# Optimization experiments

Measured on AMD Instinct MI355X. Metric: run time of the kernel, lower is better.

The kernel has to match this reference:

```python
import jax, jax.numpy as jnp
import numpy as np

B, S, T = 32, 2048, 768
NH, DH, DHID = 8, 96, 384  # num_heads, head_dim, hidden_dim=4*head_dim


def setup_inputs() -> dict:
    key = jax.random.key(0)
    k = jax.random.split(key, 7)
    token_embeddings = jax.random.normal(k[0], (B, S, T), dtype=jnp.float32)
    attention_mask = jnp.ones((B, S), dtype=jnp.float32)
    # per-head Linear params, stacked on a leading head axis (PyTorch default-ish init scale)
    P_w = jax.random.normal(k[1], (NH, T, DH), dtype=jnp.float32) * (1.0 / np.sqrt(T))
    P_b = jax.random.normal(k[2], (NH, DH), dtype=jnp.float32) * 0.01
    W1_w = jax.random.normal(k[3], (NH, DH, DHID), dtype=jnp.float32) * (1.0 / np.sqrt(DH))
    W1_b = jax.random.normal(k[4], (NH, DHID), dtype=jnp.float32) * 0.01
    W2_w = jax.random.normal(k[5], (NH, DHID, DH), dtype=jnp.float32) * (1.0 / np.sqrt(DHID))
    W2_b = jax.random.normal(k[6], (NH, DH), dtype=jnp.float32) * 0.01
    return {
        'token_embeddings': token_embeddings,
        'attention_mask': attention_mask,
        'P_w': P_w, 'P_b': P_b,
        'W1_w': W1_w, 'W1_b': W1_b,
        'W2_w': W2_w, 'W2_b': W2_b,
    }


def reference(token_embeddings, attention_mask, P_w, P_b, W1_w, W1_b, W2_w, W2_b):
    # Batched over heads instead of the original Python loop; same math per head.
    # H_i = P_i(H): (B, NH, S, DH)
    Hi = jnp.einsum('bst,htd->bhsd', token_embeddings, P_w) + P_b[None, :, None, :]
    # A_i = W2_i(relu(W1_i(H_i))): (B, NH, S, DH)
    A = jax.nn.relu(jnp.einsum('bhsd,hde->bhse', Hi, W1_w) + W1_b[None, :, None, :])
    A = jnp.einsum('bhse,hed->bhsd', A, W2_w) + W2_b[None, :, None, :]
    # masked softmax over the sequence axis (log(mask) adds -inf at padded tokens)
    log_mask = jnp.log(attention_mask)[:, None, :, None]  # (B,1,S,1)
    A = jax.nn.softmax(A + log_mask, axis=2)
    # weighted sum over tokens: (B, NH, DH)
    v = jnp.sum(Hi * A, axis=2)
    # concat heads -> (B, NH*DH) == (B, sentence_dim)
    return v.reshape(v.shape[0], NH * DH)
```

## Files before the change

kernel.cpp:

```cpp
#include <hip/hip_runtime.h>
#include <cstdint>
#include <cstddef>

#define Bsz   32
#define Ssz   2048
#define Tsz   768
#define NH    8
#define DH    96
#define DHID  384
#define Ncols (NH*DH)

using u16 = unsigned short;
typedef __bf16 bf16x8 __attribute__((ext_vector_type(8)));
typedef __bf16 bf16x4 __attribute__((ext_vector_type(4)));
typedef float  f32x4  __attribute__((ext_vector_type(4)));

__device__ __forceinline__ u16 f2bn(float f) {
  __bf16 h = (__bf16)f;
  return __builtin_bit_cast(u16, h);
}
__device__ __forceinline__ float b2f(u16 u) {
  return __builtin_bit_cast(float, (uint32_t)u << 16);
}

typedef const __attribute__((address_space(1))) void* gas_t;
typedef __attribute__((address_space(3))) void* las_t;
__device__ __forceinline__ void gload16(const void* g, void* s) {
  __builtin_amdgcn_global_load_lds((gas_t)g, (las_t)s, 16, 0, 0);
}

__global__ __launch_bounds__(256) void k_cvt(const float* __restrict__ e,
                                             u16* __restrict__ o)
{
  size_t t = (size_t)blockIdx.x * 256 + threadIdx.x;
  #pragma unroll
  for (int it = 0; it < 3; ++it) {
    size_t i = (t + (size_t)it * 2097152) * 8;
    float4 v0 = *reinterpret_cast<const float4*>(e + i);
    float4 v1 = *reinterpret_cast<const float4*>(e + i + 4);
    bf16x8 p;
    p[0] = (__bf16)v0.x; p[1] = (__bf16)v0.y; p[2] = (__bf16)v0.z; p[3] = (__bf16)v0.w;
    p[4] = (__bf16)v1.x; p[5] = (__bf16)v1.y; p[6] = (__bf16)v1.z; p[7] = (__bf16)v1.w;
    *reinterpret_cast<bf16x8*>(o + i) = p;
  }
}

__global__ __launch_bounds__(256) void k_pack(const float* __restrict__ Pw,
    const float* __restrict__ W1w, const float* __restrict__ W2w,
    u16* __restrict__ B1t, u16* __restrict__ W1t, u16* __restrict__ W2t)
{
  int i = blockIdx.x * 256 + threadIdx.x;
  if (i < 589824) {
    int n = i / 768, k = i % 768;
    int h = n / 96, d = n % 96;
    B1t[i] = f2bn(Pw[(size_t)h*73728 + (size_t)k*96 + d]);
  } else if (i < 589824 + 294912) {
    int j = i - 589824;
    int h = j / 36864, r = j % 36864;
    int n = r / 96, k = r % 96;
    W1t[j] = f2bn(W1w[(size_t)h*36864 + (size_t)k*384 + n]);
  } else if (i < 589824 + 2*294912) {
    int q = i - 589824 - 294912;
    int h = q / 36864, r = q % 36864;
    int n = r / 384, k = r % 384;
    W2t[q] = f2bn(W2w[(size_t)h*36864 + (size_t)k*96 + n]);
  }
}

__global__ __launch_bounds__(256) void k_gemm1(const u16* __restrict__ embb,
    const u16* __restrict__ B1t, const float* __restrict__ Pb, u16* __restrict__ Hi)
{
  __shared__ u16 As[128*64];
  __shared__ u16 Bs[128*64];
  const int tid  = threadIdx.x;
  const int lane = tid & 63;
  const int w    = tid >> 6;
  const int wr = w >> 1, wc = w & 1;
  const int L = blockIdx.x;
  const int widx = (L & 7) * 384 + (L >> 3);
  const int bm = widx / 6, bn = widx % 6;
  const int l15 = lane & 15, lg = lane >> 4;

  const int lrow = lane >> 3;
  const int lchk = (lane & 7) ^ lrow;

  f32x4 acc[4][4] = {};

  #pragma unroll 1
  for (int kt = 0; kt < 12; ++kt) {
    const int k0 = kt * 64;
    #pragma unroll
    for (int i = 0; i < 4; ++i) {
      const int r8 = (w*4 + i)*8;
      gload16(embb + (size_t)(bm*128 + r8 + lrow)*Tsz + k0 + lchk*8,
              &As[r8*64]);
      gload16(B1t  + (size_t)(bn*128 + r8 + lrow)*Tsz + k0 + lchk*8,
              &Bs[r8*64]);
    }
    __syncthreads();

    __builtin_amdgcn_s_setprio(1);
    #pragma unroll
    for (int kk = 0; kk < 2; ++kk) {
      const int clog = kk*4 + lg;
      bf16x8 b[4];
      #pragma unroll
      for (int c = 0; c < 4; ++c) {
        const int Rb = wc*64 + c*16 + l15;
        b[c] = *reinterpret_cast<const bf16x8*>(&Bs[Rb*64 + (clog ^ (Rb & 7))*8]);
      }
      bf16x8 a[4];
      #pragma unroll
      for (int m = 0; m < 4; ++m) {
        const int R = wr*64 + m*16 + l15;
        a[m] = *reinterpret_cast<const bf16x8*>(&As[R*64 + (clog ^ (R & 7))*8]);
      }
      #pragma unroll
      for (int m = 0; m < 4; ++m)
        #pragma unroll
        for (int c = 0; c < 4; ++c)
          acc[m][c] = __builtin_amdgcn_mfma_f32_16x16x32_bf16(a[m], b[c], acc[m][c], 0, 0, 0);
    }
    __builtin_amdgcn_s_setprio(0);
    __syncthreads();
  }

  #pragma unroll
  for (int c = 0; c < 4; ++c) {
    int col = bn*128 + wc*64 + c*16 + l15;
    float bias = Pb[col];
    #pragma unroll
    for (int m = 0; m < 4; ++m) {
      int row0 = bm*128 + wr*64 + m*16 + lg*4;
      #pragma unroll
      for (int j = 0; j < 4; ++j)
        Hi[(size_t)(row0 + j)*Ncols + col] = f2bn(acc[m][c][j] + bias);
    }
  }
}

__global__ __launch_bounds__(256, 2) void k_gemm1_fb(const float* __restrict__ emb,
    const u16* __restrict__ B1t, const float* __restrict__ Pb, u16* __restrict__ Hi)
{
  __shared__ u16 As[2][128*64];
  __shared__ u16 Bs[2][128*64];
  const int tid  = threadIdx.x;
  const int lane = tid & 63;
  const int w    = tid >> 6;
  const int wr = w >> 1, wc = w & 1;
  const int L = blockIdx.x;
  const int widx = (L & 7) * 384 + (L >> 3);
  const int bm = widx / 6, bn = widx % 6;
  const int l15 = lane & 15, lg = lane >> 4;

  const int srow   = lane >> 3;
  const int schunk = lane & 7;
  const int wchunk = schunk ^ srow;

  bf16x8 pa[4];
  bf16x8 pb[4];

  auto load_tile = [&](int kt) {
    const int k0 = kt * 64;
    #pragma unroll
    for (int i = 0; i < 4; ++i) {
      const int row = w*32 + i*8 + srow;
      const float* src = emb + (size_t)(bm*128 + row)*Tsz + k0 + schunk*8;
      float4 v0 = *reinterpret_cast<const float4*>(src);
      float4 v1 = *reinterpret_cast<const float4*>(src + 4);
      bf16x8 af;
      af[0] = (__bf16)v0.x; af[1] = (__bf16)v0.y; af[2] = (__bf16)v0.z; af[3] = (__bf16)v0.w;
      af[4] = (__bf16)v1.x; af[5] = (__bf16)v1.y; af[6] = (__bf16)v1.z; af[7] = (__bf16)v1.w;
      pa[i] = af;
    }
    #pragma unroll
    for (int i = 0; i < 4; ++i) {
      const int row = w*32 + i*8 + srow;
      pb[i] = *reinterpret_cast<const bf16x8*>(
          B1t + (size_t)(bn*128 + row)*Tsz + k0 + schunk*8);
    }
  };
  auto write_tile = [&](int buf) {
    #pragma unroll
    for (int i = 0; i < 4; ++i) {
      const int row = w*32 + i*8 + srow;
      *reinterpret_cast<bf16x8*>(&As[buf][row*64 + wchunk*8]) = pa[i];
      *reinterpret_cast<bf16x8*>(&Bs[buf][row*64 + wchunk*8]) = pb[i];
    }
  };

  f32x4 acc[4][4] = {};

  load_tile(0);
  write_tile(0);
  __syncthreads();

  #pragma unroll 1
  for (int kt = 0; kt < 12; ++kt) {
    const int cur = kt & 1;
    if (kt < 11) load_tile(kt + 1);
    __builtin_amdgcn_s_setprio(1);
    #pragma unroll
    for (int kk = 0; kk < 2; ++kk) {
      const int clog = kk*4 + lg;
      bf16x8 b[4];
      #pragma unroll
      for (int c = 0; c < 4; ++c) {
        const int Rb = wc*64 + c*16 + l15;
        b[c] = *reinterpret_cast<const bf16x8*>(&Bs[cur][Rb*64 + (clog ^ (Rb & 7))*8]);
      }
      bf16x8 a[4];
      #pragma unroll
      for (int m = 0; m < 4; ++m) {
        const int R = wr*64 + m*16 + l15;
        a[m] = *reinterpret_cast<const bf16x8*>(&As[cur][R*64 + (clog ^ (R & 7))*8]);
      }
      #pragma unroll
      for (int m = 0; m < 4; ++m)
        #pragma unroll
        for (int c = 0; c < 4; ++c)
          acc[m][c] = __builtin_amdgcn_mfma_f32_16x16x32_bf16(a[m], b[c], acc[m][c], 0, 0, 0);
    }
    __builtin_amdgcn_s_setprio(0);
    if (kt < 11) write_tile(cur ^ 1);
    __syncthreads();
  }

  #pragma unroll
  for (int c = 0; c < 4; ++c) {
    int col = bn*128 + wc*64 + c*16 + l15;
    float bias = Pb[col];
    #pragma unroll
    for (int m = 0; m < 4; ++m) {
      int row0 = bm*128 + wr*64 + m*16 + lg*4;
      #pragma unroll
      for (int j = 0; j < 4; ++j)
        Hi[(size_t)(row0 + j)*Ncols + col] = f2bn(acc[m][c][j] + bias);
    }
  }
}

__global__ __launch_bounds__(256, 1) void k_ffn_pool(
    const u16* __restrict__ Hi, const u16* __restrict__ W1t, const u16* __restrict__ W2t,
    const float* __restrict__ b1, const float* __restrict__ b2v, const float* __restrict__ mask,
    float* __restrict__ out)
{
  __shared__ u16 W1s[384][104];
  __shared__ u16 W2s[96][392];
  __shared__ u16 Zb[4][16][40];

  const int tid = threadIdx.x, lane = tid & 63, w = tid >> 6;
  const int l15 = lane & 15, lg = lane >> 4;
  const int h = blockIdx.x, b = blockIdx.y;

  const u16* W1h = W1t + (size_t)h * DHID * DH;
  const u16* W2h = W2t + (size_t)h * DH * DHID;
  const float* b1h = b1 + h * DHID;

  for (int i = tid; i < 384*12; i += 256) {
    int r = i / 12, g = i % 12;
    uint4 v = *reinterpret_cast<const uint4*>(W1h + (size_t)r*DH + g*8);
    *reinterpret_cast<uint4*>(&W1s[r][g*8]) = v;
  }
  for (int i = tid; i < 96*48; i += 256) {
    int r = i / 48, g = i % 48;
    uint4 v = *reinterpret_cast<const uint4*>(W2h + (size_t)r*DHID + g*8);
    *reinterpret_cast<uint4*>(&W2s[r][g*8]) = v;
  }
  __syncthreads();

  float b2s[6];
  #pragma unroll
  for (int ct = 0; ct < 6; ++ct) b2s[ct] = b2v[h*DH + ct*16 + l15];

  float Mr[6], Lr[6], Ar[6];
  #pragma unroll
  for (int ct = 0; ct < 6; ++ct) { Mr[ct] = -3.4e38f; Lr[ct] = 0.f; Ar[ct] = 0.f; }

  #pragma unroll 1
  for (int pass = 0; pass < 8; ++pass) {
    const size_t prow = (size_t)b*Ssz + (size_t)w*512 + (size_t)pass*64;

    bf16x8 hifr[4][3];
    #pragma unroll
    for (int s = 0; s < 4; ++s)
      #pragma unroll
      for (int ks = 0; ks < 3; ++ks)
        hifr[s][ks] = *reinterpret_cast<const bf16x8*>(
            Hi + (prow + s*16 + l15)*Ncols + h*DH + ks*32 + lg*8);

    f32x4 lgt[4][6] = {};

    #pragma unroll 2
    for (int c = 0; c < 12; ++c) {
      bf16x8 a1c[2][3];
      #pragma unroll
      for (int t = 0; t < 2; ++t)
        #pragma unroll
        for (int ks = 0; ks < 3; ++ks)
          a1c[t][ks] = *reinterpret_cast<const bf16x8*>(
              &W1s[c*32 + t*16 + l15][ks*32 + lg*8]);
      float4 bc0 = *reinterpret_cast<const float4*>(b1h + c*32 + lg*4);
      float4 bc1 = *reinterpret_cast<const float4*>(b1h + c*32 + 16 + lg*4);
      bf16x8 b2fr[6];
      #pragma unroll
      for (int ct = 0; ct < 6; ++ct)
        b2fr[ct] = *reinterpret_cast<const bf16x8*>(&W2s[ct*16 + l15][c*32 + lg*8]);

      #pragma unroll
      for (int s = 0; s < 4; ++s) {
        f32x4 z0 = {}, z1 = {};
        #pragma unroll
        for (int ks = 0; ks < 3; ++ks) {
          z0 = __builtin_amdgcn_mfma_f32_16x16x32_bf16(a1c[0][ks], hifr[s][ks], z0, 0, 0, 0);
          z1 = __builtin_amdgcn_mfma_f32_16x16x32_bf16(a1c[1][ks], hifr[s][ks], z1, 0, 0, 0);
        }
        bf16x4 p0, p1;
        p0[0] = (__bf16)fmaxf(z0[0] + bc0.x, 0.f);
        p0[1] = (__bf16)fmaxf(z0[1] + bc0.y, 0.f);
        p0[2] = (__bf16)fmaxf(z0[2] + bc0.z, 0.f);
        p0[3] = (__bf16)fmaxf(z0[3] + bc0.w, 0.f);
        p1[0] = (__bf16)fmaxf(z1[0] + bc1.x, 0.f);
        p1[1] = (__bf16)fmaxf(z1[1] + bc1.y, 0.f);
        p1[2] = (__bf16)fmaxf(z1[2] + bc1.z, 0.f);
        p1[3] = (__bf16)fmaxf(z1[3] + bc1.w, 0.f);
        *reinterpret_cast<uint2*>(&Zb[w][l15][lg*4])      = __builtin_bit_cast(uint2, p0);
        *reinterpret_cast<uint2*>(&Zb[w][l15][16 + lg*4]) = __builtin_bit_cast(uint2, p1);
        bf16x8 zf = *reinterpret_cast<const bf16x8*>(&Zb[w][l15][lg*8]);
        #pragma unroll
        for (int ct = 0; ct < 6; ++ct)
          lgt[s][ct] = __builtin_amdgcn_mfma_f32_16x16x32_bf16(zf, b2fr[ct], lgt[s][ct], 0, 0, 0);
      }
    }

    float lmv[4][4];
    #pragma unroll
    for (int s = 0; s < 4; ++s) {
      float4 mk = *reinterpret_cast<const float4*>(&mask[prow + s*16 + lg*4]);
      lmv[s][0] = __logf(mk.x); lmv[s][1] = __logf(mk.y);
      lmv[s][2] = __logf(mk.z); lmv[s][3] = __logf(mk.w);
    }
    float G[4][6][4];
    #pragma unroll
    for (int s = 0; s < 4; ++s)
      #pragma unroll
      for (int ct = 0; ct < 6; ++ct)
        #pragma unroll
        for (int j = 0; j < 4; ++j)
          G[s][ct][j] = b2f(Hi[(prow + s*16 + lg*4 + j)*Ncols + h*DH + ct*16 + l15]);

    #pragma unroll
    for (int ct = 0; ct < 6; ++ct) {
      float av[4][4];
      float m16 = -3.4e38f;
      #pragma unroll
      for (int s = 0; s < 4; ++s)
        #pragma unroll
        for (int j = 0; j < 4; ++j) {
          av[s][j] = lgt[s][ct][j] + b2s[ct] + lmv[s][j];
          m16 = fmaxf(m16, av[s][j]);
        }
      m16 = fmaxf(m16, __shfl_xor(m16, 16));
      m16 = fmaxf(m16, __shfl_xor(m16, 32));
      float l16 = 0.f, a16 = 0.f;
      #pragma unroll
      for (int s = 0; s < 4; ++s)
        #pragma unroll
        for (int j = 0; j < 4; ++j) {
          float p = __expf(av[s][j] - m16);
          l16 += p;
          a16 += p * G[s][ct][j];
        }
      l16 += __shfl_xor(l16, 16); l16 += __shfl_xor(l16, 32);
      a16 += __shfl_xor(a16, 16); a16 += __shfl_xor(a16, 32);
      float M2 = fmaxf(Mr[ct], m16);
      float eo = __expf(Mr[ct] - M2), en = __expf(m16 - M2);
      Lr[ct] = Lr[ct]*eo + l16*en;
      Ar[ct] = Ar[ct]*eo + a16*en;
      Mr[ct] = M2;
    }
  }

  float* mw = reinterpret_cast<float*>(&Zb[w][0][0]);
  if (lane < 16) {
    #pragma unroll
    for (int ct = 0; ct < 6; ++ct) {
      mw[      ct*16 + l15] = Mr[ct];
      mw[ 96 + ct*16 + l15] = Lr[ct];
      mw[192 + ct*16 + l15] = Ar[ct];
    }
  }
  __syncthreads();
  if (tid < 96) {
    const float* m0 = reinterpret_cast<const float*>(&Zb[0][0][0]);
    const float* m1 = reinterpret_cast<const float*>(&Zb[1][0][0]);
    const float* m2 = reinterpret_cast<const float*>(&Zb[2][0][0]);
    const float* m3 = reinterpret_cast<const float*>(&Zb[3][0][0]);
    float m = fmaxf(fmaxf(m0[tid], m1[tid]), fmaxf(m2[tid], m3[tid]));
    float e0 = __expf(m0[tid] - m), e1 = __expf(m1[tid] - m);
    float e2 = __expf(m2[tid] - m), e3 = __expf(m3[tid] - m);
    float l = m0[96+tid]*e0 + m1[96+tid]*e1 + m2[96+tid]*e2 + m3[96+tid]*e3;
    float a = m0[192+tid]*e0 + m1[192+tid]*e1 + m2[192+tid]*e2 + m3[192+tid]*e3;
    out[(size_t)b * Ncols + h*DH + tid] = a / l;
  }
}

extern "C" void kernel_launch(void* const* d_in, const int* in_sizes, int n_in,
                              void* d_out, int out_size, void* d_ws, size_t ws_size,
                              hipStream_t stream)
{
  const float* emb  = (const float*)d_in[0];
  const float* mask = (const float*)d_in[1];
  const float* Pw   = (const float*)d_in[2];
  const float* Pb   = (const float*)d_in[3];
  const float* W1w  = (const float*)d_in[4];
  const float* W1b  = (const float*)d_in[5];
  const float* W2w  = (const float*)d_in[6];
  const float* W2b  = (const float*)d_in[7];
  float* out = (float*)d_out;

  char* ws = (char*)d_ws;
  if (ws_size >= 203685888ull) {
    u16* embb = (u16*)(ws);
    u16* Hi   = (u16*)(ws + 100663296ull);
    u16* B1t  = (u16*)(ws + 201326592ull);
    u16* W1t  = (u16*)(ws + 202506240ull);
    u16* W2t  = (u16*)(ws + 203096064ull);
    k_cvt <<<dim3(8192), dim3(256), 0, stream>>>(emb, embb);
    k_pack<<<dim3(4608), dim3(256), 0, stream>>>(Pw, W1w, W2w, B1t, W1t, W2t);
    k_gemm1<<<dim3(3072), dim3(256), 0, stream>>>(embb, B1t, Pb, Hi);
    k_ffn_pool<<<dim3(8, 32), dim3(256), 0, stream>>>(Hi, W1t, W2t, W1b, W2b, mask, out);
  } else {
    u16* Hi  = (u16*)(ws);
    u16* B1t = (u16*)(ws + 100663296ull);
    u16* W1t = (u16*)(ws + 101842944ull);
    u16* W2t = (u16*)(ws + 102432768ull);
    k_pack<<<dim3(4608), dim3(256), 0, stream>>>(Pw, W1w, W2w, B1t, W1t, W2t);
    k_gemm1_fb<<<dim3(3072), dim3(256), 0, stream>>>(emb, B1t, Pb, Hi);
    k_ffn_pool<<<dim3(8, 32), dim3(256), 0, stream>>>(Hi, W1t, W2t, W1b, W2b, mask, out);
  }
}
```

Baseline: 286.0 us.

## Pre-swizzle FFN weights into MFMA fragment order and use eight waves per block

The packing kernel now writes W1 and W2 in the exact per-lane MFMA fragment order, so the FFN kernel loads them into LDS with flat contiguous copies and reads fragments with lane-contiguous, conflict-free accesses instead of padded row-strided ones. The FFN/pool kernel also grows from 256 to 512 threads per block, with each of 8 waves covering 256 tokens instead of 512. The online-softmax merge is widened to 8 partials. The goal is more latency hiding in this 256-block kernel and lower LDS load cost, at the price of higher register and LDS pressure per CU.

```diff
diff --git a/kernel.cpp b/kernel.cpp
--- a/kernel.cpp
+++ b/kernel.cpp
@@ -47,7 +47,7 @@
 
 __global__ __launch_bounds__(256) void k_pack(const float* __restrict__ Pw,
     const float* __restrict__ W1w, const float* __restrict__ W2w,
-    u16* __restrict__ B1t, u16* __restrict__ W1t, u16* __restrict__ W2t)
+    u16* __restrict__ B1t, u16* __restrict__ W1f, u16* __restrict__ W2f)
 {
   int i = blockIdx.x * 256 + threadIdx.x;
   if (i < 589824) {
@@ -57,13 +57,24 @@
   } else if (i < 589824 + 294912) {
     int j = i - 589824;
     int h = j / 36864, r = j % 36864;
-    int n = r / 96, k = r % 96;
-    W1t[j] = f2bn(W1w[(size_t)h*36864 + (size_t)k*384 + n]);
+    int CI = r / 8, e = r % 8;
+    int lane = CI % 64, ci2 = CI / 64;
+    int ks = ci2 % 3, ct2 = ci2 / 3;
+    int t = ct2 % 2, c = ct2 / 2;
+    int l15 = lane & 15, lg = lane >> 4;
+    int n = c*32 + t*16 + l15;
+    int k = ks*32 + lg*8 + e;
+    W1f[j] = f2bn(W1w[(size_t)h*36864 + (size_t)k*384 + n]);
   } else if (i < 589824 + 2*294912) {
     int q = i - 589824 - 294912;
     int h = q / 36864, r = q % 36864;
-    int n = r / 384, k = r % 384;
-    W2t[q] = f2bn(W2w[(size_t)h*36864 + (size_t)k*96 + n]);
+    int CI = r / 8, e = r % 8;
+    int lane = CI % 64, ci2 = CI / 64;
+    int ct = ci2 % 6, c = ci2 / 6;
+    int l15 = lane & 15, lg = lane >> 4;
+    int n = ct*16 + l15;
+    int k = c*32 + lg*8 + e;
+    W2f[q] = f2bn(W2w[(size_t)h*36864 + (size_t)k*96 + n]);
   }
 }
 
@@ -240,32 +251,26 @@
   }
 }
 
-__global__ __launch_bounds__(256, 1) void k_ffn_pool(
-    const u16* __restrict__ Hi, const u16* __restrict__ W1t, const u16* __restrict__ W2t,
+__global__ __launch_bounds__(512, 1) void k_ffn_pool(
+    const u16* __restrict__ Hi, const u16* __restrict__ W1f, const u16* __restrict__ W2f,
     const float* __restrict__ b1, const float* __restrict__ b2v, const float* __restrict__ mask,
     float* __restrict__ out)
 {
-  __shared__ u16 W1s[384][104];
-  __shared__ u16 W2s[96][392];
-  __shared__ u16 Zb[4][16][40];
+  __shared__ u16 W1s[36864];
+  __shared__ u16 W2s[36864];
+  __shared__ u16 Zb[8][16][40];
 
   const int tid = threadIdx.x, lane = tid & 63, w = tid >> 6;
   const int l15 = lane & 15, lg = lane >> 4;
   const int h = blockIdx.x, b = blockIdx.y;
 
-  const u16* W1h = W1t + (size_t)h * DHID * DH;
-  const u16* W2h = W2t + (size_t)h * DH * DHID;
+  const u16* W1h = W1f + (size_t)h * DHID * DH;
+  const u16* W2h = W2f + (size_t)h * DH * DHID;
   const float* b1h = b1 + h * DHID;
 
-  for (int i = tid; i < 384*12; i += 256) {
-    int r = i / 12, g = i % 12;
-    uint4 v = *reinterpret_cast<const uint4*>(W1h + (size_t)r*DH + g*8);
-    *reinterpret_cast<uint4*>(&W1s[r][g*8]) = v;
-  }
-  for (int i = tid; i < 96*48; i += 256) {
-    int r = i / 48, g = i % 48;
-    uint4 v = *reinterpret_cast<const uint4*>(W2h + (size_t)r*DHID + g*8);
-    *reinterpret_cast<uint4*>(&W2s[r][g*8]) = v;
+  for (int i = tid; i < 4608; i += 512) {
+    *reinterpret_cast<uint4*>(&W1s[i*8]) = *reinterpret_cast<const uint4*>(W1h + i*8);
+    *reinterpret_cast<uint4*>(&W2s[i*8]) = *reinterpret_cast<const uint4*>(W2h + i*8);
   }
   __syncthreads();
 
@@ -278,8 +283,8 @@
   for (int ct = 0; ct < 6; ++ct) { Mr[ct] = -3.4e38f; Lr[ct] = 0.f; Ar[ct] = 0.f; }
 
   #pragma unroll 1
-  for (int pass = 0; pass < 8; ++pass) {
-    const size_t prow = (size_t)b*Ssz + (size_t)w*512 + (size_t)pass*64;
+  for (int pass = 0; pass < 4; ++pass) {
+    const size_t prow = (size_t)b*Ssz + (size_t)w*256 + (size_t)pass*64;
 
     bf16x8 hifr[4][3];
     #pragma unroll
@@ -299,13 +304,14 @@
         #pragma unroll
         for (int ks = 0; ks < 3; ++ks)
           a1c[t][ks] = *reinterpret_cast<const bf16x8*>(
-              &W1s[c*32 + t*16 + l15][ks*32 + lg*8]);
+              &W1s[(((c*2 + t)*3 + ks)*64 + lane)*8]);
       float4 bc0 = *reinterpret_cast<const float4*>(b1h + c*32 + lg*4);
       float4 bc1 = *reinterpret_cast<const float4*>(b1h + c*32 + 16 + lg*4);
       bf16x8 b2fr[6];
       #pragma unroll
       for (int ct = 0; ct < 6; ++ct)
-        b2fr[ct] = *reinterpret_cast<const bf16x8*>(&W2s[ct*16 + l15][c*32 + lg*8]);
+        b2fr[ct] = *reinterpret_cast<const bf16x8*>(
+            &W2s[((c*6 + ct)*64 + lane)*8]);
 
       #pragma unroll
       for (int s = 0; s < 4; ++s) {
@@ -392,15 +398,20 @@
   }
   __syncthreads();
   if (tid < 96) {
-    const float* m0 = reinterpret_cast<const float*>(&Zb[0][0][0]);
-    const float* m1 = reinterpret_cast<const float*>(&Zb[1][0][0]);
-    const float* m2 = reinterpret_cast<const float*>(&Zb[2][0][0]);
-    const float* m3 = reinterpret_cast<const float*>(&Zb[3][0][0]);
-    float m = fmaxf(fmaxf(m0[tid], m1[tid]), fmaxf(m2[tid], m3[tid]));
-    float e0 = __expf(m0[tid] - m), e1 = __expf(m1[tid] - m);
-    float e2 = __expf(m2[tid] - m), e3 = __expf(m3[tid] - m);
-    float l = m0[96+tid]*e0 + m1[96+tid]*e1 + m2[96+tid]*e2 + m3[96+tid]*e3;
-    float a = m0[192+tid]*e0 + m1[192+tid]*e1 + m2[192+tid]*e2 + m3[192+tid]*e3;
+    float m = -3.4e38f;
+    #pragma unroll
+    for (int q = 0; q < 8; ++q) {
+      const float* mq = reinterpret_cast<const float*>(&Zb[q][0][0]);
+      m = fmaxf(m, mq[tid]);
+    }
+    float l = 0.f, a = 0.f;
+    #pragma unroll
+    for (int q = 0; q < 8; ++q) {
+      const float* mq = reinterpret_cast<const float*>(&Zb[q][0][0]);
+      float sc = __expf(mq[tid] - m);
+      l += mq[96 + tid] * sc;
+      a += mq[192 + tid] * sc;
+    }
     out[(size_t)b * Ncols + h*DH + tid] = a / l;
   }
 }
@@ -424,19 +435,19 @@
     u16* embb = (u16*)(ws);
     u16* Hi   = (u16*)(ws + 100663296ull);
     u16* B1t  = (u16*)(ws + 201326592ull);
-    u16* W1t  = (u16*)(ws + 202506240ull);
-    u16* W2t  = (u16*)(ws + 203096064ull);
+    u16* W1f  = (u16*)(ws + 202506240ull);
+    u16* W2f  = (u16*)(ws + 203096064ull);
     k_cvt <<<dim3(8192), dim3(256), 0, stream>>>(emb, embb);
-    k_pack<<<dim3(4608), dim3(256), 0, stream>>>(Pw, W1w, W2w, B1t, W1t, W2t);
+    k_pack<<<dim3(4608), dim3(256), 0, stream>>>(Pw, W1w, W2w, B1t, W1f, W2f);
     k_gemm1<<<dim3(3072), dim3(256), 0, stream>>>(embb, B1t, Pb, Hi);
-    k_ffn_pool<<<dim3(8, 32), dim3(256), 0, stream>>>(Hi, W1t, W2t, W1b, W2b, mask, out);
+    k_ffn_pool<<<dim3(8, 32), dim3(512), 0, stream>>>(Hi, W1f, W2f, W1b, W2b, mask, out);
   } else {
     u16* Hi  = (u16*)(ws);
     u16* B1t = (u16*)(ws + 100663296ull);
-    u16* W1t = (u16*)(ws + 101842944ull);
-    u16* W2t = (u16*)(ws + 102432768ull);
-    k_pack<<<dim3(4608), dim3(256), 0, stream>>>(Pw, W1w, W2w, B1t, W1t, W2t);
+    u16* W1f = (u16*)(ws + 101842944ull);
+    u16* W2f = (u16*)(ws + 102432768ull);
+    k_pack<<<dim3(4608), dim3(256), 0, stream>>>(Pw, W1w, W2w, B1t, W1f, W2f);
     k_gemm1_fb<<<dim3(3072), dim3(256), 0, stream>>>(emb, B1t, Pb, Hi);
-    k_ffn_pool<<<dim3(8, 32), dim3(256), 0, stream>>>(Hi, W1t, W2t, W1b, W2b, mask, out);
-  }
-}
+    k_ffn_pool<<<dim3(8, 32), dim3(512), 0, stream>>>(Hi, W1f, W2f, W1b, W2b, mask, out);
+  }
+}
```

Measured after the change: 254.5 us. 11.0% less time.
